# Performance work log

Measured on AMD Instinct MI355X. Metric: run time of the kernel, lower is better.

The kernel has to match this reference:

```python
import jax, jax.numpy as jnp
import numpy as np

B = 4096      # batch
D = 256       # flattened input feature dim
NUMFEAT = 1 + D + D * (D + 1) // 2  # 33153: bias + linear + quadratic terms


def setup_inputs() -> dict:
    key = jax.random.key(0)
    k1, k2 = jax.random.split(key)
    x = jax.random.normal(k1, (B, D), dtype=jnp.float32)
    # nn.Linear(numfeat, 10, bias=False): weight shape (10, numfeat)
    W = jax.random.normal(k2, (10, NUMFEAT), dtype=jnp.float32) * 0.01
    return {"x": x, "W": W}


def reference(x, W):
    # x: (B, D) -- original does x.view(B, -1); already 2D here.
    b, d = x.shape
    # sklearn PolynomialFeatures(degree=2) column order:
    # [1, x_0..x_{d-1}, x_0*x_0, x_0*x_1, ..., x_{d-1}*x_{d-1}]
    # i.e. combinations_with_replacement == upper-triangular (incl. diagonal)
    iu0, iu1 = np.triu_indices(d)  # static index constants
    ones = jnp.ones((b, 1), dtype=x.dtype)
    cross = x[:, iu0] * x[:, iu1]          # (B, D*(D+1)/2)
    feats = jnp.concatenate([ones, x, cross], axis=1)  # (B, NUMFEAT)
    return feats @ W.T                      # (B, 10)
```

## Files before the change

kernel.cpp:

```cpp
#include <hip/hip_runtime.h>


#define DD 256
#define NF 33153
#define BM 64
#define BK 64
#define TPB 256
#define APAD 72

typedef __attribute__((ext_vector_type(8))) short short8;
typedef __attribute__((ext_vector_type(4))) float floatx4;
typedef __attribute__((ext_vector_type(4))) unsigned short ushortx4;

__device__ inline unsigned short f2bf(float f) {
    unsigned u = __builtin_bit_cast(unsigned, f);
    return (unsigned short)((u + 0x7FFFu + ((u >> 16) & 1u)) >> 16);
}

__global__ void xconv_kernel(const float* __restrict__ x, unsigned short* __restrict__ xb) {
    int i = (blockIdx.x * TPB + threadIdx.x) * 4;
    float4 v = *(const float4*)&x[i];
    ushortx4 r;
    r.x = f2bf(v.x); r.y = f2bf(v.y); r.z = f2bf(v.z); r.w = f2bf(v.w);
    *(ushortx4*)&xb[i] = r;
}

__global__ void gbuild_kernel(const float* __restrict__ W, unsigned short* __restrict__ G) {
    int oi = blockIdx.x;
    int o = oi >> 8, i = oi & 255;
    int j = threadIdx.x;
    int base = o * NF + 257 + i * DD - (i * (i - 1)) / 2 - i;
    float v = (j >= i) ? W[base + j] : 0.f;
    G[oi * DD + j] = f2bf(v);
}

__global__ __launch_bounds__(TPB)
void PolynomialRegression_75385265979710_kernel(const float* __restrict__ x,
                                                const float* __restrict__ W,
                                                const unsigned short* __restrict__ Xbf,
                                                const unsigned short* __restrict__ G,
                                                float* __restrict__ out) {
    __shared__ __align__(16) unsigned short As[BM * APAD];
    __shared__ float red[4 * BM];

    const int tid  = threadIdx.x;
    const int lane = tid & 63;
    const int wave = tid >> 6;
    const int ln   = lane & 15;
    const int quad = lane >> 4;
    const int rowbase = blockIdx.x * BM;
    const int o  = blockIdx.y;
    const int wn0 = wave * 64;

    floatx4 acc[4][4];
#pragma unroll
    for (int mt = 0; mt < 4; ++mt)
#pragma unroll
        for (int nt = 0; nt < 4; ++nt) acc[mt][nt] = (floatx4)0.f;

    for (int kt = 0; kt < 4; ++kt) {
        const int k0 = kt * BK;
#pragma unroll
        for (int p = 0; p < 2; ++p) {
            int c = p * TPB + tid;
            int r = c >> 3, col = (c & 7) * 8;
            *(short8*)&As[r * APAD + col] =
                *(const short8*)&Xbf[(rowbase + r) * DD + k0 + col];
        }
        __syncthreads();
#pragma unroll
        for (int ks = 0; ks < 2; ++ks) {
            const int kk = k0 + ks * 32 + quad * 8;
            short8 b[4], a[4];
#pragma unroll
            for (int nt = 0; nt < 4; ++nt)
                b[nt] = *(const short8*)&G[(o * DD + wn0 + nt * 16 + ln) * DD + kk];
#pragma unroll
            for (int mt = 0; mt < 4; ++mt)
                a[mt] = *(const short8*)&As[(mt * 16 + ln) * APAD + ks * 32 + quad * 8];
#pragma unroll
            for (int mt = 0; mt < 4; ++mt)
#pragma unroll
                for (int nt = 0; nt < 4; ++nt)
                    acc[mt][nt] = __builtin_amdgcn_mfma_f32_16x16x32_bf16(
                        a[mt], b[nt], acc[mt][nt], 0, 0, 0);
        }
        __syncthreads();
    }

    float wl[4];
#pragma unroll
    for (int nt = 0; nt < 4; ++nt)
        wl[nt] = W[o * NF + 1 + wn0 + nt * 16 + ln];

#pragma unroll
    for (int mt = 0; mt < 4; ++mt) {
#pragma unroll
        for (int r = 0; r < 4; ++r) {
            const int m = mt * 16 + quad * 4 + r;
            float p = 0.f;
#pragma unroll
            for (int nt = 0; nt < 4; ++nt) {
                float xv = x[(rowbase + m) * DD + wn0 + nt * 16 + ln];
                p = fmaf(xv, acc[mt][nt][r] + wl[nt], p);
            }
            p += __shfl_xor(p, 1);
            p += __shfl_xor(p, 2);
            p += __shfl_xor(p, 4);
            p += __shfl_xor(p, 8);
            if (ln == 0) red[wave * BM + m] = p;
        }
    }
    __syncthreads();

    if (tid < BM) {
        const int m = tid;
        float s = red[m] + red[BM + m] + red[2 * BM + m] + red[3 * BM + m] + W[o * NF];
        out[(rowbase + m) * 10 + o] = s;
    }
}

extern "C" void kernel_launch(void* const* d_in, const int* in_sizes, int n_in,
                              void* d_out, int out_size, void* d_ws, size_t ws_size,
                              hipStream_t stream) {
    const float* x = (const float*)d_in[0];
    const float* W = (const float*)d_in[1];
    float* out = (float*)d_out;

    unsigned short* Xbf = (unsigned short*)d_ws;
    unsigned short* G   = Xbf + 4096 * DD;

    xconv_kernel<<<4096 * DD / (4 * TPB), TPB, 0, stream>>>(x, Xbf);
    gbuild_kernel<<<10 * DD, TPB, 0, stream>>>(W, G);

    dim3 grid(4096 / BM, 10);
    PolynomialRegression_75385265979710_kernel<<<grid, TPB, 0, stream>>>(x, W, Xbf, G, out);
}
```

Measured before the change: 79.02 us.

## Fuse prep kernels, skip zero triangle of G, and accumulate with atomics

Merges the x-conversion and G-building kernels into one prep launch, which also writes the bias into the output. The GEMM is retiled to 128x128 blocks with two blocks per output along the i dimension. The upper-half block starts its K loop at 128 because the lower triangle of G is zero there, removing about a quarter of the MFMA work. LDS staging and the block reduction are dropped: operands are read directly from global memory and partial sums go to the output with atomicAdd. This adds atomic contention and nondeterministic summation order, and it relies on the prep kernel finishing its output initialisation before the GEMM runs.

Result: slower. 90.20 us (+14.2%).

```diff
diff --git a/kernel.cpp b/kernel.cpp
--- a/kernel.cpp
+++ b/kernel.cpp
@@ -3,10 +3,7 @@
 
 #define DD 256
 #define NF 33153
-#define BM 64
-#define BK 64
 #define TPB 256
-#define APAD 72
 
 typedef __attribute__((ext_vector_type(8))) short short8;
 typedef __attribute__((ext_vector_type(4))) float floatx4;
@@ -17,21 +14,28 @@
     return (unsigned short)((u + 0x7FFFu + ((u >> 16) & 1u)) >> 16);
 }
 
-__global__ void xconv_kernel(const float* __restrict__ x, unsigned short* __restrict__ xb) {
-    int i = (blockIdx.x * TPB + threadIdx.x) * 4;
-    float4 v = *(const float4*)&x[i];
-    ushortx4 r;
-    r.x = f2bf(v.x); r.y = f2bf(v.y); r.z = f2bf(v.z); r.w = f2bf(v.w);
-    *(ushortx4*)&xb[i] = r;
-}
-
-__global__ void gbuild_kernel(const float* __restrict__ W, unsigned short* __restrict__ G) {
-    int oi = blockIdx.x;
-    int o = oi >> 8, i = oi & 255;
-    int j = threadIdx.x;
-    int base = o * NF + 257 + i * DD - (i * (i - 1)) / 2 - i;
-    float v = (j >= i) ? W[base + j] : 0.f;
-    G[oi * DD + j] = f2bf(v);
+__global__ __launch_bounds__(TPB)
+void prep_kernel(const float* __restrict__ x, const float* __restrict__ W,
+                 unsigned short* __restrict__ Xbf, unsigned short* __restrict__ G,
+                 float* __restrict__ out) {
+    int b = blockIdx.x;
+    if (b < 1024) {
+        int i = (b * TPB + threadIdx.x) * 4;
+        float4 v = *(const float4*)&x[i];
+        ushortx4 r;
+        r.x = f2bf(v.x); r.y = f2bf(v.y); r.z = f2bf(v.z); r.w = f2bf(v.w);
+        *(ushortx4*)&Xbf[i] = r;
+    } else if (b < 1024 + 2560) {
+        int oi = b - 1024;
+        int o = oi >> 8, i = oi & 255;
+        int j = threadIdx.x;
+        int base = o * NF + 257 + i * DD - (i * (i - 1)) / 2 - i;
+        float v = (j >= i) ? W[base + j] : 0.f;
+        G[oi * DD + j] = f2bf(v);
+    } else {
+        int e = (b - 3584) * TPB + threadIdx.x;
+        out[e] = W[(e % 10) * NF];
+    }
 }
 
 __global__ __launch_bounds__(TPB)
@@ -40,17 +44,25 @@
                                                 const unsigned short* __restrict__ Xbf,
                                                 const unsigned short* __restrict__ G,
                                                 float* __restrict__ out) {
-    __shared__ __align__(16) unsigned short As[BM * APAD];
-    __shared__ float red[4 * BM];
-
     const int tid  = threadIdx.x;
     const int lane = tid & 63;
-    const int wave = tid >> 6;
     const int ln   = lane & 15;
     const int quad = lane >> 4;
-    const int rowbase = blockIdx.x * BM;
-    const int o  = blockIdx.y;
-    const int wn0 = wave * 64;
+    const int wave = tid >> 6;
+    const int mw = wave & 1, nw = wave >> 1;
+    const int mb = blockIdx.x, nb = blockIdx.y;
+    const int o = nb >> 1, ihalf = nb & 1;
+    const int m0 = mb * 128 + mw * 64;
+    const int n0 = nb * 128 + nw * 64;
+    const int i0 = ihalf * 128 + nw * 64;
+
+    const unsigned short* ap[4];
+    const unsigned short* bp[4];
+#pragma unroll
+    for (int t = 0; t < 4; ++t) {
+        ap[t] = Xbf + (m0 + t * 16 + ln) * DD + quad * 8;
+        bp[t] = G   + (n0 + t * 16 + ln) * DD + quad * 8;
+    }
 
     floatx4 acc[4][4];
 #pragma unroll
@@ -58,65 +70,47 @@
 #pragma unroll
         for (int nt = 0; nt < 4; ++nt) acc[mt][nt] = (floatx4)0.f;
 
-    for (int kt = 0; kt < 4; ++kt) {
-        const int k0 = kt * BK;
-#pragma unroll
-        for (int p = 0; p < 2; ++p) {
-            int c = p * TPB + tid;
-            int r = c >> 3, col = (c & 7) * 8;
-            *(short8*)&As[r * APAD + col] =
-                *(const short8*)&Xbf[(rowbase + r) * DD + k0 + col];
-        }
-        __syncthreads();
-#pragma unroll
-        for (int ks = 0; ks < 2; ++ks) {
-            const int kk = k0 + ks * 32 + quad * 8;
-            short8 b[4], a[4];
-#pragma unroll
-            for (int nt = 0; nt < 4; ++nt)
-                b[nt] = *(const short8*)&G[(o * DD + wn0 + nt * 16 + ln) * DD + kk];
-#pragma unroll
-            for (int mt = 0; mt < 4; ++mt)
-                a[mt] = *(const short8*)&As[(mt * 16 + ln) * APAD + ks * 32 + quad * 8];
-#pragma unroll
-            for (int mt = 0; mt < 4; ++mt)
-#pragma unroll
-                for (int nt = 0; nt < 4; ++nt)
-                    acc[mt][nt] = __builtin_amdgcn_mfma_f32_16x16x32_bf16(
-                        a[mt], b[nt], acc[mt][nt], 0, 0, 0);
-        }
-        __syncthreads();
+#define KSTEP(kt) { \
+        const int kk = (kt) * 32; \
+        short8 a[4], b[4]; \
+        _Pragma("unroll") for (int t = 0; t < 4; ++t) a[t] = *(const short8*)(ap[t] + kk); \
+        _Pragma("unroll") for (int t = 0; t < 4; ++t) b[t] = *(const short8*)(bp[t] + kk); \
+        _Pragma("unroll") for (int mt = 0; mt < 4; ++mt) \
+        _Pragma("unroll") for (int nt = 0; nt < 4; ++nt) \
+            acc[mt][nt] = __builtin_amdgcn_mfma_f32_16x16x32_bf16(a[mt], b[nt], acc[mt][nt], 0, 0, 0); \
     }
 
-    float wl[4];
+    if (ihalf == 0) {
+#pragma unroll
+        for (int kt = 0; kt < 8; ++kt) KSTEP(kt)
+    } else {
+#pragma unroll
+        for (int kt = 4; kt < 8; ++kt) KSTEP(kt)
+    }
+#undef KSTEP
+
+    float w1[4];
 #pragma unroll
     for (int nt = 0; nt < 4; ++nt)
-        wl[nt] = W[o * NF + 1 + wn0 + nt * 16 + ln];
+        w1[nt] = W[o * NF + 1 + i0 + nt * 16 + ln];
 
 #pragma unroll
     for (int mt = 0; mt < 4; ++mt) {
 #pragma unroll
         for (int r = 0; r < 4; ++r) {
-            const int m = mt * 16 + quad * 4 + r;
+            const int m = m0 + mt * 16 + quad * 4 + r;
             float p = 0.f;
 #pragma unroll
             for (int nt = 0; nt < 4; ++nt) {
-                float xv = x[(rowbase + m) * DD + wn0 + nt * 16 + ln];
-                p = fmaf(xv, acc[mt][nt][r] + wl[nt], p);
+                float xv = x[m * DD + i0 + nt * 16 + ln];
+                p = fmaf(xv, acc[mt][nt][r] + w1[nt], p);
             }
             p += __shfl_xor(p, 1);
             p += __shfl_xor(p, 2);
             p += __shfl_xor(p, 4);
             p += __shfl_xor(p, 8);
-            if (ln == 0) red[wave * BM + m] = p;
+            if (ln == 0) atomicAdd(&out[m * 10 + o], p);
         }
-    }
-    __syncthreads();
-
-    if (tid < BM) {
-        const int m = tid;
-        float s = red[m] + red[BM + m] + red[2 * BM + m] + red[3 * BM + m] + W[o * NF];
-        out[(rowbase + m) * 10 + o] = s;
     }
 }
 
@@ -130,9 +124,8 @@
     unsigned short* Xbf = (unsigned short*)d_ws;
     unsigned short* G   = Xbf + 4096 * DD;
 
-    xconv_kernel<<<4096 * DD / (4 * TPB), TPB, 0, stream>>>(x, Xbf);
-    gbuild_kernel<<<10 * DD, TPB, 0, stream>>>(W, G);
+    prep_kernel<<<1024 + 2560 + 160, TPB, 0, stream>>>(x, W, Xbf, G, out);
 
-    dim3 grid(4096 / BM, 10);
+    dim3 grid(4096 / 128, 20);
     PolynomialRegression_75385265979710_kernel<<<grid, TPB, 0, stream>>>(x, W, Xbf, G, out);
 }
```

## Fuse x bf16 conversion into main kernel and skip zero triangular K tiles

Applied to the files above, without the earlier changes.

Drops the separate x-to-bf16 conversion kernel. Each block now converts its 64x256 x tile straight into shared memory in one pass, which removes the per-K-tile syncs and the global round-trip through the workspace. Each wave skips K tiles that lie below its row range, because those entries of the upper-triangular G matrix are zero, so the MFMA work and G loads shrink. In exchange, the shared-memory footprint grows, the launch bounds hint now asks for 3 blocks per SM, and the skip leaves work unevenly spread across the waves in a block.

New measurement: 73.58 us. 1.07x faster.

```diff
diff --git a/kernel.cpp b/kernel.cpp
--- a/kernel.cpp
+++ b/kernel.cpp
@@ -4,28 +4,19 @@
 #define DD 256
 #define NF 33153
 #define BM 64
-#define BK 64
 #define TPB 256
-#define APAD 72
+#define ASTRIDE 264
 
 typedef __attribute__((ext_vector_type(8))) short short8;
 typedef __attribute__((ext_vector_type(4))) float floatx4;
-typedef __attribute__((ext_vector_type(4))) unsigned short ushortx4;
 
 __device__ inline unsigned short f2bf(float f) {
     unsigned u = __builtin_bit_cast(unsigned, f);
     return (unsigned short)((u + 0x7FFFu + ((u >> 16) & 1u)) >> 16);
 }
 
-__global__ void xconv_kernel(const float* __restrict__ x, unsigned short* __restrict__ xb) {
-    int i = (blockIdx.x * TPB + threadIdx.x) * 4;
-    float4 v = *(const float4*)&x[i];
-    ushortx4 r;
-    r.x = f2bf(v.x); r.y = f2bf(v.y); r.z = f2bf(v.z); r.w = f2bf(v.w);
-    *(ushortx4*)&xb[i] = r;
-}
-
-__global__ void gbuild_kernel(const float* __restrict__ W, unsigned short* __restrict__ G) {
+__global__ __launch_bounds__(TPB)
+void gbuild_kernel(const float* __restrict__ W, unsigned short* __restrict__ G) {
     int oi = blockIdx.x;
     int o = oi >> 8, i = oi & 255;
     int j = threadIdx.x;
@@ -34,13 +25,12 @@
     G[oi * DD + j] = f2bf(v);
 }
 
-__global__ __launch_bounds__(TPB)
+__global__ __launch_bounds__(TPB, 3)
 void PolynomialRegression_75385265979710_kernel(const float* __restrict__ x,
                                                 const float* __restrict__ W,
-                                                const unsigned short* __restrict__ Xbf,
                                                 const unsigned short* __restrict__ G,
                                                 float* __restrict__ out) {
-    __shared__ __align__(16) unsigned short As[BM * APAD];
+    __shared__ __align__(16) unsigned short As[BM * ASTRIDE];
     __shared__ float red[4 * BM];
 
     const int tid  = threadIdx.x;
@@ -49,8 +39,23 @@
     const int ln   = lane & 15;
     const int quad = lane >> 4;
     const int rowbase = blockIdx.x * BM;
-    const int o  = blockIdx.y;
+    const int o   = blockIdx.y;
     const int wn0 = wave * 64;
+
+#pragma unroll
+    for (int it = 0; it < 8; ++it) {
+        int idx = it * 2048 + tid * 8;
+        int r = idx >> 8, c = idx & 255;
+        float4 v0 = *(const float4*)&x[(rowbase + r) * DD + c];
+        float4 v1 = *(const float4*)&x[(rowbase + r) * DD + c + 4];
+        short8 p;
+        p[0] = (short)f2bf(v0.x); p[1] = (short)f2bf(v0.y);
+        p[2] = (short)f2bf(v0.z); p[3] = (short)f2bf(v0.w);
+        p[4] = (short)f2bf(v1.x); p[5] = (short)f2bf(v1.y);
+        p[6] = (short)f2bf(v1.z); p[7] = (short)f2bf(v1.w);
+        *(short8*)&As[r * ASTRIDE + c] = p;
+    }
+    __syncthreads();
 
     floatx4 acc[4][4];
 #pragma unroll
@@ -58,40 +63,38 @@
 #pragma unroll
         for (int nt = 0; nt < 4; ++nt) acc[mt][nt] = (floatx4)0.f;
 
+    const unsigned short* bp[4];
+#pragma unroll
+    for (int t = 0; t < 4; ++t)
+        bp[t] = G + (o * DD + wn0 + t * 16 + ln) * DD + quad * 8;
+
+#pragma unroll
     for (int kt = 0; kt < 4; ++kt) {
-        const int k0 = kt * BK;
+        if (kt >= wave) {
 #pragma unroll
-        for (int p = 0; p < 2; ++p) {
-            int c = p * TPB + tid;
-            int r = c >> 3, col = (c & 7) * 8;
-            *(short8*)&As[r * APAD + col] =
-                *(const short8*)&Xbf[(rowbase + r) * DD + k0 + col];
-        }
-        __syncthreads();
-#pragma unroll
-        for (int ks = 0; ks < 2; ++ks) {
-            const int kk = k0 + ks * 32 + quad * 8;
-            short8 b[4], a[4];
-#pragma unroll
-            for (int nt = 0; nt < 4; ++nt)
-                b[nt] = *(const short8*)&G[(o * DD + wn0 + nt * 16 + ln) * DD + kk];
-#pragma unroll
-            for (int mt = 0; mt < 4; ++mt)
-                a[mt] = *(const short8*)&As[(mt * 16 + ln) * APAD + ks * 32 + quad * 8];
-#pragma unroll
-            for (int mt = 0; mt < 4; ++mt)
+            for (int ks = 0; ks < 2; ++ks) {
+                const int kk = kt * 64 + ks * 32;
+                short8 a[4], b[4];
 #pragma unroll
                 for (int nt = 0; nt < 4; ++nt)
-                    acc[mt][nt] = __builtin_amdgcn_mfma_f32_16x16x32_bf16(
-                        a[mt], b[nt], acc[mt][nt], 0, 0, 0);
+                    b[nt] = *(const short8*)(bp[nt] + kk);
+#pragma unroll
+                for (int mt = 0; mt < 4; ++mt)
+                    a[mt] = *(const short8*)&As[(mt * 16 + ln) * ASTRIDE + kk + quad * 8];
+#pragma unroll
+                for (int mt = 0; mt < 4; ++mt)
+#pragma unroll
+                    for (int nt = 0; nt < 4; ++nt)
+                        acc[mt][nt] = __builtin_amdgcn_mfma_f32_16x16x32_bf16(
+                            a[mt], b[nt], acc[mt][nt], 0, 0, 0);
+            }
         }
-        __syncthreads();
     }
 
-    float wl[4];
+    float w1[4];
 #pragma unroll
     for (int nt = 0; nt < 4; ++nt)
-        wl[nt] = W[o * NF + 1 + wn0 + nt * 16 + ln];
+        w1[nt] = W[o * NF + 1 + wn0 + nt * 16 + ln];
 
 #pragma unroll
     for (int mt = 0; mt < 4; ++mt) {
@@ -102,7 +105,7 @@
 #pragma unroll
             for (int nt = 0; nt < 4; ++nt) {
                 float xv = x[(rowbase + m) * DD + wn0 + nt * 16 + ln];
-                p = fmaf(xv, acc[mt][nt][r] + wl[nt], p);
+                p = fmaf(xv, acc[mt][nt][r] + w1[nt], p);
             }
             p += __shfl_xor(p, 1);
             p += __shfl_xor(p, 2);
@@ -127,12 +130,10 @@
     const float* W = (const float*)d_in[1];
     float* out = (float*)d_out;
 
-    unsigned short* Xbf = (unsigned short*)d_ws;
-    unsigned short* G   = Xbf + 4096 * DD;
+    unsigned short* G = (unsigned short*)d_ws;
 
-    xconv_kernel<<<4096 * DD / (4 * TPB), TPB, 0, stream>>>(x, Xbf);
     gbuild_kernel<<<10 * DD, TPB, 0, stream>>>(W, G);
 
     dim3 grid(4096 / BM, 10);
-    PolynomialRegression_75385265979710_kernel<<<grid, TPB, 0, stream>>>(x, W, Xbf, G, out);
+    PolynomialRegression_75385265979710_kernel<<<grid, TPB, 0, stream>>>(x, W, G, out);
 }
```
